# Kernel tuning notes

Hardware: AMD Instinct MI355X
Metric: run time of the kernel (lower is better)

## Reference

```python
import jax, jax.numpy as jnp
import numpy as np

NEG = -1e30  # finite stand-in for -inf (safe for grads)


def setup_inputs() -> dict:
    key = jax.random.key(0)
    k1, k2, k3 = jax.random.split(key, 3)
    B, T, C, L = 128, 128, 6625, 25
    predicts = jax.random.normal(k1, (B, T, C), dtype=jnp.float32)
    labels = jax.random.randint(k2, (B, L), 1, C, dtype=jnp.int32)  # blank=0 excluded
    label_lengths = jax.random.randint(k3, (B,), 1, L + 1, dtype=jnp.int32)
    return {"predicts": predicts, "labels": labels, "label_lengths": label_lengths}


def _ctc_loss(log_probs, labels, label_lengths):
    # log_probs: [T, B, C]; labels: [B, L]; full input lengths = T (as in original module)
    T, B, C = log_probs.shape
    L = labels.shape[1]
    S = 2 * L + 1  # extended label sequence: blank interleaved, blank=0
    ext = jnp.zeros((B, S), dtype=labels.dtype).at[:, 1::2].set(labels)
    # emission log-probs gathered at extended labels: [T, B, S]
    emit = jnp.take_along_axis(log_probs, jnp.broadcast_to(ext[None, :, :], (T, B, S)), axis=2)
    # skip (s-2 -> s) allowed only when ext[s] != ext[s-2] (blanks never skip)
    skip = jnp.concatenate([jnp.zeros((B, 2), dtype=bool), ext[:, 2:] != ext[:, :-2]], axis=1)

    alpha0 = jnp.full((B, S), NEG, dtype=log_probs.dtype)
    alpha0 = alpha0.at[:, 0].set(emit[0, :, 0]).at[:, 1].set(emit[0, :, 1])

    pad1 = jnp.full((B, 1), NEG, dtype=log_probs.dtype)
    pad2 = jnp.full((B, 2), NEG, dtype=log_probs.dtype)

    def step(alpha, emit_t):
        a1 = jnp.concatenate([pad1, alpha[:, :-1]], axis=1)
        a2 = jnp.where(skip, jnp.concatenate([pad2, alpha[:, :-2]], axis=1), NEG)
        m = jnp.maximum(jnp.maximum(alpha, a1), a2)
        new = m + jnp.log(jnp.exp(alpha - m) + jnp.exp(a1 - m) + jnp.exp(a2 - m)) + emit_t
        return new, None

    alphaT, _ = jax.lax.scan(step, alpha0, emit[1:])
    idx_last = (2 * label_lengths)[:, None]  # final blank position
    ll = jnp.logaddexp(
        jnp.take_along_axis(alphaT, idx_last, axis=1)[:, 0],
        jnp.take_along_axis(alphaT, idx_last - 1, axis=1)[:, 0],
    )
    loss = -ll
    loss = jnp.where(loss > 1e29, 0.0, loss)  # zero_infinity=True
    # reduction='mean': per-sample loss divided by target length, then batch mean
    return jnp.mean(loss / label_lengths.astype(loss.dtype))


def reference(predicts, labels, label_lengths):
    B = predicts.shape[0]
    log_probs = jax.nn.log_softmax(jnp.transpose(predicts, (1, 0, 2)), axis=-1)  # [T,B,C]
    loss = _ctc_loss(log_probs, labels, label_lengths) / B  # module divides again by B
    return loss
```

## Files before the change

kernel.cpp:

```cpp
#include <hip/hip_runtime.h>
#include <math.h>


#define NEGV (-1e30f)

constexpr int Bc = 128;
constexpr int Tc = 128;
constexpr int Cc = 6625;
constexpr int Lc = 25;
constexpr int Sc = 2 * Lc + 1;

__global__ __launch_bounds__(256) void k_emit(const float* __restrict__ predicts,
                                              const int* __restrict__ labels,
                                              float* __restrict__ emit) {
    const int row = blockIdx.x;
    const int b = row / Tc;
    const float* __restrict__ x = predicts + (size_t)row * Cc;
    const int tid = threadIdx.x;

    float m = NEGV, s = 0.f;
    for (int i = tid; i < Cc; i += 256) {
        float v = x[i];
        if (v > m) {
            s = s * __expf(m - v) + 1.f;
            m = v;
        } else {
            s += __expf(v - m);
        }
    }
    for (int off = 32; off; off >>= 1) {
        float mo = __shfl_xor(m, off);
        float so = __shfl_xor(s, off);
        float M = fmaxf(m, mo);
        s = s * __expf(m - M) + so * __expf(mo - M);
        m = M;
    }
    __shared__ float sm[4], ss[4];
    __shared__ float lse_sh;
    const int wave = tid >> 6, lane = tid & 63;
    if (lane == 0) { sm[wave] = m; ss[wave] = s; }
    __syncthreads();
    if (tid == 0) {
        float M = sm[0], Ssum = ss[0];
        for (int w = 1; w < 4; ++w) {
            float M2 = fmaxf(M, sm[w]);
            Ssum = Ssum * __expf(M - M2) + ss[w] * __expf(sm[w] - M2);
            M = M2;
        }
        lse_sh = M + __logf(Ssum);
    }
    __syncthreads();
    if (tid < Sc) {
        int c = (tid & 1) ? labels[b * Lc + (tid >> 1)] : 0;
        emit[(size_t)row * Sc + tid] = x[c] - lse_sh;
    }
}

__global__ __launch_bounds__(64) void k_ctc(const float* __restrict__ emit,
                                            const int* __restrict__ labels,
                                            const int* __restrict__ lens,
                                            float* __restrict__ out) {
    const int b = blockIdx.x;
    const int s = threadIdx.x;

    const int ext = (s < Sc && (s & 1)) ? labels[b * Lc + (s >> 1)] : 0;
    const int ext_m2 = __shfl_up(ext, 2);
    const bool skip = (s >= 2) && (s < Sc) && (ext != ext_m2);

    const float* __restrict__ eb = emit + (size_t)b * Tc * Sc;

    float alpha = NEGV;
    if (s == 0) alpha = eb[0];
    else if (s == 1) alpha = eb[1];

    for (int t = 1; t < Tc; ++t) {
        float a1 = __shfl_up(alpha, 1);
        if (s < 1) a1 = NEGV;
        float a2 = __shfl_up(alpha, 2);
        if (!skip) a2 = NEGV;
        float m = fmaxf(fmaxf(alpha, a1), a2);
        float e = (s < Sc) ? eb[t * Sc + s] : NEGV;
        alpha = m + __logf(__expf(alpha - m) + __expf(a1 - m) + __expf(a2 - m)) + e;
    }

    const int len = lens[b];
    const int idx = 2 * len;
    const float ahi = __shfl(alpha, idx);
    const float alo = __shfl(alpha, idx - 1);
    if (s == 0) {
        float mm = fmaxf(ahi, alo);
        float ll = mm + __logf(__expf(ahi - mm) + __expf(alo - mm));
        float loss = -ll;
        if (loss > 1e29f) loss = 0.f;
        atomicAdd(out, loss / ((float)len * (float)Bc * (float)Bc));
    }
}

extern "C" void kernel_launch(void* const* d_in, const int* in_sizes, int n_in,
                              void* d_out, int out_size, void* d_ws, size_t ws_size,
                              hipStream_t stream) {
    const float* predicts = (const float*)d_in[0];
    const int* labels = (const int*)d_in[1];
    const int* lens = (const int*)d_in[2];
    float* out = (float*)d_out;
    float* emit = (float*)d_ws;

    hipMemsetAsync(out, 0, sizeof(float), stream);
    k_emit<<<Bc * Tc, 256, 0, stream>>>(predicts, labels, emit);
    k_ctc<<<Bc, 64, 0, stream>>>(emit, labels, lens, out);
}
```

Baseline: 655.6 us.

## Register-cache rows with float4 loads and two-pass softmax; prefetch CTC emissions

The emission kernel now loads each 6625-float row into registers with aligned float4 loads, handling a misaligned prologue and a tail separately. It then computes the row max and the exp-sum in two passes, replacing the per-element online-softmax rescaling and its compound shuffle reduction. The CTC recurrence prefetches the next timestep's emission value to hide load latency inside the serial loop. The cost is higher register pressure from 7 float4 values per thread and extra barriers.

```diff
diff --git a/kernel.cpp b/kernel.cpp
--- a/kernel.cpp
+++ b/kernel.cpp
@@ -1,5 +1,6 @@
 #include <hip/hip_runtime.h>
 #include <math.h>
+#include <stdint.h>
 
 
 #define NEGV (-1e30f)
@@ -9,50 +10,75 @@
 constexpr int Cc = 6625;
 constexpr int Lc = 25;
 constexpr int Sc = 2 * Lc + 1;
+constexpr int VPT = 7;
 
 __global__ __launch_bounds__(256) void k_emit(const float* __restrict__ predicts,
                                               const int* __restrict__ labels,
                                               float* __restrict__ emit) {
     const int row = blockIdx.x;
-    const int b = row / Tc;
+    const int b = row >> 7;
     const float* __restrict__ x = predicts + (size_t)row * Cc;
     const int tid = threadIdx.x;
 
-    float m = NEGV, s = 0.f;
-    for (int i = tid; i < Cc; i += 256) {
-        float v = x[i];
-        if (v > m) {
-            s = s * __expf(m - v) + 1.f;
-            m = v;
-        } else {
-            s += __expf(v - m);
+    const int mis = (int)(((uintptr_t)x >> 2) & 3);
+    const int npro = (4 - mis) & 3;
+    const int nvec = (Cc - npro) >> 2;
+    const int ntail = (Cc - npro) & 3;
+    const float4* __restrict__ xv = (const float4*)(x + npro);
+    const int tbase = npro + (nvec << 2);
+
+    float4 vals[VPT];
+    float pval = NEGV, tval = NEGV;
+    if (tid < npro) pval = x[tid];
+    if (tid < ntail) tval = x[tbase + tid];
+#pragma unroll
+    for (int k = 0; k < VPT; ++k) {
+        int j = tid + (k << 8);
+        if (j < nvec) vals[k] = xv[j];
+    }
+
+    float m = fmaxf(pval, tval);
+#pragma unroll
+    for (int k = 0; k < VPT; ++k) {
+        int j = tid + (k << 8);
+        if (j < nvec) {
+            float4 v = vals[k];
+            m = fmaxf(m, fmaxf(fmaxf(v.x, v.y), fmaxf(v.z, v.w)));
         }
     }
-    for (int off = 32; off; off >>= 1) {
-        float mo = __shfl_xor(m, off);
-        float so = __shfl_xor(s, off);
-        float M = fmaxf(m, mo);
-        s = s * __expf(m - M) + so * __expf(mo - M);
-        m = M;
+    for (int off = 32; off; off >>= 1) m = fmaxf(m, __shfl_xor(m, off));
+
+    __shared__ float sh[4];
+    __shared__ float bc;
+    const int wave = tid >> 6, lane = tid & 63;
+    if (lane == 0) sh[wave] = m;
+    __syncthreads();
+    if (tid == 0) bc = fmaxf(fmaxf(sh[0], sh[1]), fmaxf(sh[2], sh[3]));
+    __syncthreads();
+    const float M = bc;
+
+    float ssum = 0.f;
+    if (tid < npro) ssum += __expf(pval - M);
+    if (tid < ntail) ssum += __expf(tval - M);
+#pragma unroll
+    for (int k = 0; k < VPT; ++k) {
+        int j = tid + (k << 8);
+        if (j < nvec) {
+            float4 v = vals[k];
+            ssum += __expf(v.x - M) + __expf(v.y - M) + __expf(v.z - M) + __expf(v.w - M);
+        }
     }
-    __shared__ float sm[4], ss[4];
-    __shared__ float lse_sh;
-    const int wave = tid >> 6, lane = tid & 63;
-    if (lane == 0) { sm[wave] = m; ss[wave] = s; }
+    for (int off = 32; off; off >>= 1) ssum += __shfl_xor(ssum, off);
     __syncthreads();
-    if (tid == 0) {
-        float M = sm[0], Ssum = ss[0];
-        for (int w = 1; w < 4; ++w) {
-            float M2 = fmaxf(M, sm[w]);
-            Ssum = Ssum * __expf(M - M2) + ss[w] * __expf(sm[w] - M2);
-            M = M2;
-        }
-        lse_sh = M + __logf(Ssum);
-    }
+    if (lane == 0) sh[wave] = ssum;
     __syncthreads();
+    if (tid == 0) bc = M + __logf(sh[0] + sh[1] + sh[2] + sh[3]);
+    __syncthreads();
+    const float lse = bc;
+
     if (tid < Sc) {
         int c = (tid & 1) ? labels[b * Lc + (tid >> 1)] : 0;
-        emit[(size_t)row * Sc + tid] = x[c] - lse_sh;
+        emit[(size_t)row * Sc + tid] = x[c] - lse;
     }
 }
 
@@ -73,14 +99,16 @@
     if (s == 0) alpha = eb[0];
     else if (s == 1) alpha = eb[1];
 
+    float e = (s < Sc) ? eb[Sc + s] : NEGV;
     for (int t = 1; t < Tc; ++t) {
+        float e_next = (t + 1 < Tc && s < Sc) ? eb[(t + 1) * Sc + s] : NEGV;
         float a1 = __shfl_up(alpha, 1);
         if (s < 1) a1 = NEGV;
         float a2 = __shfl_up(alpha, 2);
         if (!skip) a2 = NEGV;
         float m = fmaxf(fmaxf(alpha, a1), a2);
-        float e = (s < Sc) ? eb[t * Sc + s] : NEGV;
         alpha = m + __logf(__expf(alpha - m) + __expf(a1 - m) + __expf(a2 - m)) + e;
+        e = e_next;
     }
 
     const int len = lens[b];
```

New measurement: 583.7 us. -11.0%, faster.
